# Performance work log

Hardware: AMD Instinct MI355X
Metric: run time of the kernel (lower is better)

Reference implementation:

```python
import jax, jax.numpy as jnp
import numpy as np

D = 300
L = 5
NUM_ATOMS = 87  # MASK_ATOM_ID + 1
BN_EPS = 1e-5


def setup_inputs() -> dict:
    key = jax.random.key(0)
    ks = jax.random.split(key, 24)
    N, E, G = 100000, 250000, 4096
    s = 0.05
    inp = {
        'z': jax.random.randint(ks[0], (N,), 0, 86),
        'chirality': jax.random.uniform(ks[1], (N,), jnp.float32),
        'formal_charge': jax.random.normal(ks[2], (N,), jnp.float32),
        'edge_index': jax.random.randint(ks[3], (2, E), 0, N),
        'edge_attr': jax.random.normal(ks[4], (E, 3), jnp.float32),
        'batch': jnp.sort(jax.random.randint(ks[5], (N,), 0, G)),
        'num_graphs': G,
        # parameters
        'atom_emb': jax.random.normal(ks[6], (NUM_ATOMS, D), jnp.float32) * s,
        'nW1': jax.random.normal(ks[7], (2, D), jnp.float32) * s,
        'nb1': jnp.zeros((D,), jnp.float32),
        'nW2': jax.random.normal(ks[8], (D, D), jnp.float32) * s,
        'nb2': jnp.zeros((D,), jnp.float32),
        'eW1': jax.random.normal(ks[9], (3, D), jnp.float32) * s,
        'eb1': jnp.zeros((D,), jnp.float32),
        'eW2': jax.random.normal(ks[10], (D, D), jnp.float32) * s,
        'eb2': jnp.zeros((D,), jnp.float32),
        'mW1': jax.random.normal(ks[11], (L, D, D), jnp.float32) * s,
        'mb1': jnp.zeros((L, D), jnp.float32),
        'mW2': jax.random.normal(ks[12], (L, D, D), jnp.float32) * s,
        'mb2': jnp.zeros((L, D), jnp.float32),
        'gamma': jnp.ones((L, D), jnp.float32),
        'beta': jnp.zeros((L, D), jnp.float32),
        'pW': jax.random.normal(ks[13], (D, D), jnp.float32) * s,
        'pb': jnp.zeros((D,), jnp.float32),
    }
    return inp


def _mlp2(x, W1, b1, W2, b2):
    return jax.nn.relu(x @ W1 + b1) @ W2 + b2


def reference(z, chirality, formal_charge, edge_index, edge_attr, batch, num_graphs,
              atom_emb, nW1, nb1, nW2, nb2, eW1, eb1, eW2, eb2,
              mW1, mb1, mW2, mb2, gamma, beta, pW, pb):
    N = z.shape[0]
    # node features: atom embedding + projected (chirality, formal_charge)
    node_attr = jnp.stack([chirality, formal_charge], axis=-1)  # [N,2]
    x = atom_emb[z] + _mlp2(node_attr, nW1, nb1, nW2, nb2)      # [N,D]
    # edge features: encode 3-d bond attrs to D (edge_proj is Identity since dims match)
    e = _mlp2(edge_attr, eW1, eb1, eW2, eb2)                    # [E,D]
    src, dst = edge_index[0], edge_index[1]
    h = x
    for l in range(L):
        # GINEConv: mlp((1+eps)*x_i + sum_j relu(x_j + e_ij)), eps=0
        msg = jax.nn.relu(h[src] + e)                           # [E,D] gather
        agg = jax.ops.segment_sum(msg, dst, num_segments=N)     # [N,D] scatter-add
        h2 = _mlp2(h + agg, mW1[l], mb1[l], mW2[l], mb2[l])
        # BatchNorm1d (training stats over nodes, biased var)
        mu = jnp.mean(h2, axis=0)
        var = jnp.var(h2, axis=0)
        h2 = (h2 - mu) * jax.lax.rsqrt(var + BN_EPS) * gamma[l] + beta[l]
        h = jax.nn.relu(h2)
    # per-graph mean pooling
    sums = jax.ops.segment_sum(h, batch, num_segments=num_graphs)      # [G,D]
    counts = jax.ops.segment_sum(jnp.ones((N,), h.dtype), batch, num_segments=num_graphs)
    pooled = sums / jnp.maximum(counts, 1.0)[:, None]
    return pooled @ pW + pb
```

## Files before the change

### kernel.cpp

```cpp
#include <hip/hip_runtime.h>

#define DD 300
#define KP 320
#define WTR 384

typedef __attribute__((ext_vector_type(8))) short short8v;
typedef __attribute__((ext_vector_type(4))) float f32x4;

__device__ __forceinline__ float4 ld4(const float* p) { return *(const float4*)p; }

__device__ __forceinline__ unsigned short f2bf(float f) {
    unsigned int u = __float_as_uint(f);
    unsigned int r = (u + 0x7fffu + ((u >> 16) & 1u)) >> 16;
    return (unsigned short)r;
}
__device__ __forceinline__ float bf2f(unsigned short b) {
    return __uint_as_float(((unsigned int)b) << 16);
}

__device__ __forceinline__ void gload16(const void* g, void* l) {
    __builtin_amdgcn_global_load_lds(
        (const __attribute__((address_space(1))) unsigned int*)g,
        (__attribute__((address_space(3))) unsigned int*)l, 16, 0, 0);
}

__device__ __forceinline__ unsigned char f2e4(float f) {
    unsigned int u = __float_as_uint(f);
    unsigned int s = (u >> 24) & 0x80u;
    float a = __uint_as_float(u & 0x7fffffffu);
    if (a >= 448.f) return (unsigned char)(s | 0x7Eu);
    if (a < 0x1p-10f) return (unsigned char)s;
    int e = (int)((__float_as_uint(a) >> 23) & 0xFF) - 127;
    int q = (e >= -6) ? (e - 3) : -9;
    float scale = __uint_as_float((unsigned int)(127 - q) << 23);
    int m = __float2int_rn(a * scale);
    if (e >= -6) {
        if (m == 16) { m = 8; e += 1; }
        return (unsigned char)(s | ((unsigned int)(e + 7) << 3) | (unsigned int)(m - 8));
    } else {
        if (m == 8) return (unsigned char)(s | (1u << 3));
        return (unsigned char)(s | (unsigned int)m);
    }
}
__device__ __forceinline__ float e42f(unsigned char b) {
    unsigned int s = ((unsigned int)(b & 0x80u)) << 24;
    unsigned int ef = (b >> 3) & 0xFu, mf = b & 7u;
    float mag = (ef == 0) ? ((float)mf) * 0x1p-9f
                          : __uint_as_float(((ef + 120u) << 23) | (mf << 20));
    return __uint_as_float(__float_as_uint(mag) | s);
}

__global__ void prep_all(const float* __restrict__ nW2, const float* __restrict__ eW2,
                         const float* __restrict__ mW1, const float* __restrict__ mW2,
                         unsigned short* __restrict__ wt,
                         double* __restrict__ bnsum, double* __restrict__ bnsq)
{
    const int per = WTR * KP;
    int id = blockIdx.x * 256 + threadIdx.x;
    if (id < 12 * per) {
        int m = id / per, r = id - m * per;
        int col = r / KP, k = r - col * KP;
        const float* W = (m == 0) ? nW2 : (m == 1) ? eW2
                       : (m < 7) ? (mW1 + (size_t)(m - 2) * DD * DD)
                                 : (mW2 + (size_t)(m - 7) * DD * DD);
        float v = (col < DD && k < DD) ? W[(size_t)k * DD + col] : 0.f;
        unsigned short h = f2bf(v);
        wt[(size_t)m * 2 * per + (size_t)col * KP + k] = h;
        wt[(size_t)m * 2 * per + per + (size_t)col * KP + k] = f2bf(v - bf2f(h));
    } else if (id < 12 * per + DD) {
        int c = id - 12 * per;
        bnsum[c] = 0.0; bnsq[c] = 0.0;
    }
}

enum { MA_DMA2 = 0, MA_BF16 = 1, MA_NODE = 2, MA_EDGE = 3 };
enum { ME_RELU = 0, ME_BN = 1, ME_EMB = 2, ME_FP8 = 3 };

constexpr int TM = 256;
constexpr int TN = 128;
constexpr int TK = 32;
constexpr int KSTEPS = 10;

template<int AM, int EM>
__launch_bounds__(512)
__global__ void mgemm(const unsigned short* __restrict__ Aa,
                      const unsigned short* __restrict__ Ab,
                      const unsigned short* __restrict__ Bth,
                      const unsigned short* __restrict__ Btl,
                      const float* __restrict__ bias,
                      const float* __restrict__ W1,
                      const float* __restrict__ b1,
                      const int* __restrict__ zidx,
                      const float* __restrict__ emb,
                      const int* __restrict__ permpos,
                      void* __restrict__ Cv,
                      double* __restrict__ bnsum, double* __restrict__ bnsq,
                      int M)
{
    constexpr bool VSTAGE = (AM == MA_NODE || AM == MA_EDGE);
    constexpr bool ALO    = (AM == MA_NODE);
    constexpr int  AP     = VSTAGE ? 40 : 32;
    __shared__ unsigned short sAh[TM * AP];
    __shared__ unsigned short sBh[TN * 32];
    __shared__ unsigned short sBl[TN * 32];
    __shared__ unsigned short sA2[(AM == MA_DMA2) ? TM * 32 : 64];
    __shared__ unsigned short sAl[ALO ? TM * 40 : 64];

    const int t    = threadIdx.x;
    const int col0 = blockIdx.x * TN;
    const int row0 = blockIdx.y * TM;
    const int lane = t & 63;
    const int wid  = t >> 6;
    const int wr   = wid >> 1;
    const int wc   = wid & 1;
    const int lr   = lane & 15;
    const int lk   = lane >> 4;

    const int arow = t >> 1;
    const int akq  = (t & 1) * 16;
    const int dmarow = lane >> 2;
    const int dmakq  = (lane & 3) * 8;
    const int wbA  = wid * 32;
    const int wbB  = wid * 16;

    const int ga = row0 + arow;
    float f0 = 0.f, f1 = 0.f, f2 = 0.f;
    if (AM == MA_NODE && ga < M) {
        f0 = ((const float*)Aa)[ga]; f1 = ((const float*)Ab)[ga];
    }
    if (AM == MA_EDGE && ga < M) {
        const float* Af = (const float*)Aa;
        f0 = Af[(size_t)ga * 3 + 0];
        f1 = Af[(size_t)ga * 3 + 1];
        f2 = Af[(size_t)ga * 3 + 2];
    }

    f32x4 acc[4][4];
#pragma unroll
    for (int i = 0; i < 4; ++i)
#pragma unroll
        for (int j = 0; j < 4; ++j) acc[i][j] = (f32x4){0.f, 0.f, 0.f, 0.f};

    for (int ks = 0; ks < KSTEPS; ++ks) {
        const int k0 = ks * TK;
        __syncthreads();

        gload16(Bth + (size_t)(col0 + wbB + dmarow) * KP + k0 + dmakq, &sBh[wbB * 32]);
        gload16(Btl + (size_t)(col0 + wbB + dmarow) * KP + k0 + dmakq, &sBl[wbB * 32]);

        if (AM == MA_DMA2) {
#pragma unroll
            for (int i = 0; i < 2; ++i) {
                const int rb = wbA + i * 16;
                gload16(Aa + (size_t)(row0 + rb + dmarow) * DD + k0 + dmakq, &sAh[rb * 32]);
                gload16(Ab + (size_t)(row0 + rb + dmarow) * DD + k0 + dmakq, &sA2[rb * 32]);
            }
        } else if (AM == MA_BF16) {
#pragma unroll
            for (int i = 0; i < 2; ++i) {
                const int rb = wbA + i * 16;
                gload16(Aa + (size_t)(row0 + rb + dmarow) * DD + k0 + dmakq, &sAh[rb * 32]);
            }
        } else {
            float v[16];
#pragma unroll
            for (int q = 0; q < 4; ++q) {
                const int k = k0 + akq + q * 4;
                if (ga < M && k < DD) {
                    float4 w0 = ld4(W1 + k);
                    float4 w1 = ld4(W1 + DD + k);
                    float4 bb = ld4(b1 + k);
                    if (AM == MA_NODE) {
                        v[q*4+0] = fmaxf(fmaf(f0, w0.x, fmaf(f1, w1.x, bb.x)), 0.f);
                        v[q*4+1] = fmaxf(fmaf(f0, w0.y, fmaf(f1, w1.y, bb.y)), 0.f);
                        v[q*4+2] = fmaxf(fmaf(f0, w0.z, fmaf(f1, w1.z, bb.z)), 0.f);
                        v[q*4+3] = fmaxf(fmaf(f0, w0.w, fmaf(f1, w1.w, bb.w)), 0.f);
                    } else {
                        float4 w2 = ld4(W1 + 2 * DD + k);
                        v[q*4+0] = fmaxf(f0*w0.x + f1*w1.x + f2*w2.x + bb.x, 0.f);
                        v[q*4+1] = fmaxf(f0*w0.y + f1*w1.y + f2*w2.y + bb.y, 0.f);
                        v[q*4+2] = fmaxf(f0*w0.z + f1*w1.z + f2*w2.z + bb.z, 0.f);
                        v[q*4+3] = fmaxf(f0*w0.w + f1*w1.w + f2*w2.w + bb.w, 0.f);
                    }
                } else {
                    v[q*4+0] = v[q*4+1] = v[q*4+2] = v[q*4+3] = 0.f;
                }
            }
#pragma unroll
            for (int q = 0; q < 4; ++q) {
                ushort4 hi;
                hi.x = f2bf(v[q*4+0]);
                hi.y = f2bf(v[q*4+1]);
                hi.z = f2bf(v[q*4+2]);
                hi.w = f2bf(v[q*4+3]);
                *(ushort4*)&sAh[arow * AP + akq + q * 4] = hi;
                if constexpr (ALO) {
                    ushort4 lo;
                    lo.x = f2bf(v[q*4+0] - bf2f(hi.x));
                    lo.y = f2bf(v[q*4+1] - bf2f(hi.y));
                    lo.z = f2bf(v[q*4+2] - bf2f(hi.z));
                    lo.w = f2bf(v[q*4+3] - bf2f(hi.w));
                    *(ushort4*)&sAl[arow * 40 + akq + q * 4] = lo;
                }
            }
        }
        __syncthreads();

        short8v aH[4], aX[4], bH[4], bL[4];
#pragma unroll
        for (int f = 0; f < 4; ++f) {
            aH[f] = *(const short8v*)&sAh[(wr * 64 + f * 16 + lr) * AP + lk * 8];
            bH[f] = *(const short8v*)&sBh[(wc * 64 + f * 16 + lr) * 32 + lk * 8];
            bL[f] = *(const short8v*)&sBl[(wc * 64 + f * 16 + lr) * 32 + lk * 8];
            if constexpr (AM == MA_DMA2)
                aX[f] = *(const short8v*)&sA2[(wr * 64 + f * 16 + lr) * 32 + lk * 8];
            if constexpr (ALO)
                aX[f] = *(const short8v*)&sAl[(wr * 64 + f * 16 + lr) * 40 + lk * 8];
        }
#pragma unroll
        for (int fi = 0; fi < 4; ++fi)
#pragma unroll
            for (int fj = 0; fj < 4; ++fj) {
                acc[fi][fj] = __builtin_amdgcn_mfma_f32_16x16x32_bf16(aH[fi], bH[fj], acc[fi][fj], 0, 0, 0);
                acc[fi][fj] = __builtin_amdgcn_mfma_f32_16x16x32_bf16(aH[fi], bL[fj], acc[fi][fj], 0, 0, 0);
                if constexpr (AM == MA_DMA2) {
                    acc[fi][fj] = __builtin_amdgcn_mfma_f32_16x16x32_bf16(aX[fi], bH[fj], acc[fi][fj], 0, 0, 0);
                    acc[fi][fj] = __builtin_amdgcn_mfma_f32_16x16x32_bf16(aX[fi], bL[fj], acc[fi][fj], 0, 0, 0);
                }
                if constexpr (ALO)
                    acc[fi][fj] = __builtin_amdgcn_mfma_f32_16x16x32_bf16(aX[fi], bH[fj], acc[fi][fj], 0, 0, 0);
            }
    }

    float csum[4], csq[4];
#pragma unroll
    for (int j = 0; j < 4; ++j) { csum[j] = 0.f; csq[j] = 0.f; }

#pragma unroll
    for (int fi = 0; fi < 4; ++fi) {
#pragma unroll
        for (int i = 0; i < 4; ++i) {
            const int r = row0 + wr * 64 + fi * 16 + lk * 4 + i;
            if (r < M) {
                int zr = 0, pr = 0;
                if (EM == ME_EMB) zr = zidx[r];
                if (EM == ME_FP8) pr = permpos[r];
#pragma unroll
                for (int fj = 0; fj < 4; ++fj) {
                    const int c = col0 + wc * 64 + fj * 16 + lr;
                    if (c < DD) {
                        float v = acc[fi][fj][i] + bias[c];
                        if (EM == ME_RELU) v = fmaxf(v, 0.f);
                        if (EM == ME_EMB)  v += emb[(size_t)zr * DD + c];
                        if (EM == ME_FP8)
                            ((unsigned char*)Cv)[(size_t)pr * DD + c] = f2e4(v);
                        else
                            ((unsigned short*)Cv)[(size_t)r * DD + c] = f2bf(v);
                        if (EM == ME_BN) { csum[fj] += v; csq[fj] += v * v; }
                    }
                }
            }
        }
    }

    if (EM == ME_BN) {
#pragma unroll
        for (int fj = 0; fj < 4; ++fj) {
            csum[fj] += __shfl_xor(csum[fj], 16);
            csum[fj] += __shfl_xor(csum[fj], 32);
            csq[fj]  += __shfl_xor(csq[fj], 16);
            csq[fj]  += __shfl_xor(csq[fj], 32);
        }
        float* sRed = (float*)sAh;
        __syncthreads();
        if (lk == 0) {
#pragma unroll
            for (int fj = 0; fj < 4; ++fj)
                sRed[wr * TN + wc * 64 + fj * 16 + lr] = csum[fj];
        }
        __syncthreads();
        if (t < TN) {
            float s = sRed[t] + sRed[TN + t] + sRed[2 * TN + t] + sRed[3 * TN + t];
            const int c = col0 + t;
            if (c < DD) unsafeAtomicAdd(&bnsum[c], (double)s);
        }
        __syncthreads();
        if (lk == 0) {
#pragma unroll
            for (int fj = 0; fj < 4; ++fj)
                sRed[wr * TN + wc * 64 + fj * 16 + lr] = csq[fj];
        }
        __syncthreads();
        if (t < TN) {
            float s = sRed[t] + sRed[TN + t] + sRed[2 * TN + t] + sRed[3 * TN + t];
            const int c = col0 + t;
            if (c < DD) unsafeAtomicAdd(&bnsq[c], (double)s);
        }
    }
}

constexpr int GBM = 128;
constexpr int GBN = 128;
constexpr int GBK = 8;
constexpr int KPAD = 304;

__launch_bounds__(256)
__global__ void gemm_final(const float* __restrict__ Aa, const float* __restrict__ Bw,
                           const float* __restrict__ bias, float* __restrict__ C, int M)
{
    __shared__ float smem[2 * GBK * GBM];
    float* As = smem;
    float* Bs = smem + GBK * GBM;

    const int t    = threadIdx.x;
    const int tx   = t & 15;
    const int ty   = t >> 4;
    const int col0 = blockIdx.x * GBN;
    const int row0 = blockIdx.y * GBM;
    const int arow = t >> 1;
    const int akq  = (t & 1) << 2;
    const int brow = t >> 5;
    const int bnq  = (t & 31) << 2;
    const int ga   = row0 + arow;
    const int gb   = col0 + bnq;

    float acc[8][8];
#pragma unroll
    for (int i = 0; i < 8; ++i)
#pragma unroll
        for (int j = 0; j < 8; ++j) acc[i][j] = 0.f;

    for (int k0 = 0; k0 < KPAD; k0 += GBK) {
        float4 av = make_float4(0.f, 0.f, 0.f, 0.f);
        const int ka = k0 + akq;
        if (ga < M && ka < DD) av = ld4(Aa + (size_t)ga * DD + ka);
        As[(akq + 0) * GBM + arow] = av.x;
        As[(akq + 1) * GBM + arow] = av.y;
        As[(akq + 2) * GBM + arow] = av.z;
        As[(akq + 3) * GBM + arow] = av.w;

        float4 bv = make_float4(0.f, 0.f, 0.f, 0.f);
        const int kb = k0 + brow;
        if (kb < DD && gb < DD) bv = ld4(Bw + (size_t)kb * DD + gb);
        *(float4*)(Bs + brow * GBN + bnq) = bv;

        __syncthreads();
#pragma unroll
        for (int kk = 0; kk < GBK; ++kk) {
            float a[8], b[8];
            *(float4*)&a[0] = *(const float4*)(As + kk * GBM + 8 * ty);
            *(float4*)&a[4] = *(const float4*)(As + kk * GBM + 8 * ty + 4);
            *(float4*)&b[0] = *(const float4*)(Bs + kk * GBN + 8 * tx);
            *(float4*)&b[4] = *(const float4*)(Bs + kk * GBN + 8 * tx + 4);
#pragma unroll
            for (int i = 0; i < 8; ++i)
#pragma unroll
                for (int j = 0; j < 8; ++j)
                    acc[i][j] = fmaf(a[i], b[j], acc[i][j]);
        }
        __syncthreads();
    }

#pragma unroll
    for (int i = 0; i < 8; ++i) {
        const int r = row0 + 8 * ty + i;
        if (r < M) {
#pragma unroll
            for (int jq = 0; jq < 2; ++jq) {
                const int c = col0 + 8 * tx + 4 * jq;
                if (c < DD) {
                    float4 bb = ld4(bias + c);
                    *(float4*)(C + (size_t)r * DD + c) = make_float4(
                        acc[i][4*jq+0] + bb.x, acc[i][4*jq+1] + bb.y,
                        acc[i][4*jq+2] + bb.z, acc[i][4*jq+3] + bb.w);
                }
            }
        }
    }
}

__global__ void deg_kernel(const int* __restrict__ dst, int* __restrict__ deg, int E)
{
    int e = blockIdx.x * 256 + threadIdx.x;
    if (e < E) atomicAdd(&deg[dst[e]], 1);
}

__global__ void scan1(const int* __restrict__ deg, int* __restrict__ out,
                      int* __restrict__ bsum, int n)
{
    __shared__ int sh[256];
    const int t = threadIdx.x;
    const int base = blockIdx.x * 1024 + t * 4;
    int v0 = (base + 0 < n) ? deg[base + 0] : 0;
    int v1 = (base + 1 < n) ? deg[base + 1] : 0;
    int v2 = (base + 2 < n) ? deg[base + 2] : 0;
    int v3 = (base + 3 < n) ? deg[base + 3] : 0;
    const int s = v0 + v1 + v2 + v3;
    sh[t] = s;
    __syncthreads();
    for (int off = 1; off < 256; off <<= 1) {
        int x = (t >= off) ? sh[t - off] : 0;
        __syncthreads();
        sh[t] += x;
        __syncthreads();
    }
    int ex = sh[t] - s;
    if (base + 0 < n) out[base + 0] = ex; ex += v0;
    if (base + 1 < n) out[base + 1] = ex; ex += v1;
    if (base + 2 < n) out[base + 2] = ex; ex += v2;
    if (base + 3 < n) out[base + 3] = ex;
    if (t == 255) bsum[blockIdx.x] = sh[255];
}

__global__ void scan2(int* __restrict__ bsum, int nb, int* __restrict__ offs, int n, int E)
{
    __shared__ int sh[256];
    const int t = threadIdx.x;
    const int v = (t < nb) ? bsum[t] : 0;
    sh[t] = v;
    __syncthreads();
    for (int off = 1; off < 256; off <<= 1) {
        int x = (t >= off) ? sh[t - off] : 0;
        __syncthreads();
        sh[t] += x;
        __syncthreads();
    }
    if (t < nb) bsum[t] = sh[t] - v;
    if (t == 0) offs[n] = E;
}

__global__ void scan3(int* __restrict__ offs, const int* __restrict__ bsum,
                      int* __restrict__ cursor, int n)
{
    int i = blockIdx.x * 256 + threadIdx.x;
    if (i < n) {
        int v = offs[i] + bsum[i >> 10];
        offs[i] = v;
        cursor[i] = v;
    }
}

__global__ void fill_kernel(const int* __restrict__ src, const int* __restrict__ dst,
                            int* __restrict__ cursor, int* __restrict__ esrc,
                            int* __restrict__ permpos, int E)
{
    int e = blockIdx.x * 256 + threadIdx.x;
    if (e < E) {
        int d = dst[e];
        int pos = atomicAdd(&cursor[d], 1);
        esrc[pos] = src[e];
        permpos[e] = pos;
    }
}

__global__ void agg_kernel(const unsigned short* __restrict__ h,
                           const unsigned char* __restrict__ e,
                           const int* __restrict__ esrc, const int* __restrict__ offs,
                           unsigned short* __restrict__ agg, int N)
{
    const int node = blockIdx.x * 4 + (threadIdx.x >> 6);
    if (node >= N) return;
    const int lane = threadIdx.x & 63;
    const int beg = offs[node], end = offs[node + 1];
    for (int q = lane; q < 75; q += 64) {
        float4 s = make_float4(0.f, 0.f, 0.f, 0.f);
        for (int p = beg; p < end; ++p) {
            const int src = esrc[p];
            ushort4 hu = *(const ushort4*)(h + (size_t)src * DD + 4 * q);
            unsigned int eu = *(const unsigned int*)(e + (size_t)p * DD + 4 * q);
            s.x += fmaxf(bf2f(hu.x) + e42f((unsigned char)(eu & 0xFF)), 0.f);
            s.y += fmaxf(bf2f(hu.y) + e42f((unsigned char)((eu >> 8) & 0xFF)), 0.f);
            s.z += fmaxf(bf2f(hu.z) + e42f((unsigned char)((eu >> 16) & 0xFF)), 0.f);
            s.w += fmaxf(bf2f(hu.w) + e42f((unsigned char)(eu >> 24)), 0.f);
        }
        *(ushort4*)(agg + (size_t)node * DD + 4 * q) =
            make_ushort4(f2bf(s.x), f2bf(s.y), f2bf(s.z), f2bf(s.w));
    }
}

__global__ void bn_fin(double* __restrict__ bnsum, double* __restrict__ bnsq,
                       const float* __restrict__ gamma, const float* __restrict__ beta,
                       float* __restrict__ scale, float* __restrict__ shift, double invN)
{
    const int c = threadIdx.x;
    if (c < DD) {
        double mu = bnsum[c] * invN;
        double var = bnsq[c] * invN - mu * mu;
        double inv = 1.0 / sqrt(var + 1e-5);
        double g = (double)gamma[c];
        scale[c] = (float)(g * inv);
        shift[c] = (float)((double)beta[c] - mu * inv * g);
        bnsum[c] = 0.0;
        bnsq[c]  = 0.0;
    }
}

__global__ void bn_apply(const unsigned short* __restrict__ h2,
                         const float* __restrict__ scale, const float* __restrict__ shift,
                         unsigned short* __restrict__ h, int total4)
{
    int idx = blockIdx.x * 256 + threadIdx.x;
    if (idx >= total4) return;
    int q = idx % 75;
    ushort4 v4 = ((const ushort4*)h2)[idx];
    float4 sc = ld4(scale + 4 * q);
    float4 sh = ld4(shift + 4 * q);
    float r0 = fmaxf(fmaf(bf2f(v4.x), sc.x, sh.x), 0.f);
    float r1 = fmaxf(fmaf(bf2f(v4.y), sc.y, sh.y), 0.f);
    float r2 = fmaxf(fmaf(bf2f(v4.z), sc.z, sh.z), 0.f);
    float r3 = fmaxf(fmaf(bf2f(v4.w), sc.w, sh.w), 0.f);
    ((ushort4*)h)[idx] = make_ushort4(f2bf(r0), f2bf(r1), f2bf(r2), f2bf(r3));
}

__global__ void pool_kernel(const unsigned short* __restrict__ h, const int* __restrict__ batch,
                            float* __restrict__ pooled, int N)
{
    const int g = blockIdx.x;
    __shared__ int sb[2];
    if (threadIdx.x == 0) {
        int lo = 0, hi = N;
        while (lo < hi) { int m = (lo + hi) >> 1; if (batch[m] < g) lo = m + 1; else hi = m; }
        sb[0] = lo;
        lo = 0; hi = N;
        while (lo < hi) { int m = (lo + hi) >> 1; if (batch[m] < g + 1) lo = m + 1; else hi = m; }
        sb[1] = lo;
    }
    __syncthreads();
    const int beg = sb[0], end = sb[1];
    const float cnt = (float)(end - beg);
    for (int d = threadIdx.x; d < DD; d += 256) {
        float s = 0.f;
        for (int i = beg; i < end; ++i) s += bf2f(h[(size_t)i * DD + d]);
        pooled[(size_t)g * DD + d] = (end > beg) ? (s / cnt) : 0.f;
    }
}

__global__ void diag_fill(float* __restrict__ out, int n, float v)
{
    int i = blockIdx.x * 256 + threadIdx.x;
    if (i < n) out[i] = v;
}

extern "C" void kernel_launch(void* const* d_in, const int* in_sizes, int n_in,
                              void* d_out, int out_size, void* d_ws, size_t ws_size,
                              hipStream_t stream)
{
    const int N = in_sizes[0];
    const int E = in_sizes[3] / 2;
    const int G = out_size / DD;
    const int NPAD = (N + 255) & ~255;

    const int*   z     = (const int*)d_in[0];
    const float* chir  = (const float*)d_in[1];
    const float* fc    = (const float*)d_in[2];
    const int*   eidx  = (const int*)d_in[3];
    const float* eattr = (const float*)d_in[4];
    const int*   batch = (const int*)d_in[5];
    const float* aemb  = (const float*)d_in[7];
    const float* nW1   = (const float*)d_in[8];
    const float* nb1   = (const float*)d_in[9];
    const float* nW2   = (const float*)d_in[10];
    const float* nb2   = (const float*)d_in[11];
    const float* eW1   = (const float*)d_in[12];
    const float* eb1   = (const float*)d_in[13];
    const float* eW2   = (const float*)d_in[14];
    const float* eb2   = (const float*)d_in[15];
    const float* mW1   = (const float*)d_in[16];
    const float* mb1   = (const float*)d_in[17];
    const float* mW2   = (const float*)d_in[18];
    const float* mb2   = (const float*)d_in[19];
    const float* gamma = (const float*)d_in[20];
    const float* beta  = (const float*)d_in[21];
    const float* pW    = (const float*)d_in[22];
    const float* pb    = (const float*)d_in[23];
    float* out = (float*)d_out;

    size_t base = 0;
    auto A = [&](size_t b) -> size_t {
        size_t r = base; base += (b + 255) & ~(size_t)255; return r;
    };
    const size_t o_h    = A((size_t)NPAD * DD * 2 + 128);
    const size_t o_t    = A((size_t)NPAD * DD * 2 + 128);
    const size_t o_g    = A((size_t)NPAD * DD * 2 + 128);
    const size_t o_bns  = A(DD * 8);
    const size_t o_bnq  = A(DD * 8);
    const size_t o_scl  = A(DD * 4);
    const size_t o_shf  = A(DD * 4);
    const size_t o_offs = A((size_t)(N + 1) * 4);
    const size_t o_cur  = A((size_t)N * 4);
    const size_t o_bsum = A(1024 * 4);
    const size_t o_src  = A((size_t)E * 4);
    const size_t o_perm = A((size_t)E * 4);
    const size_t o_wt   = A((size_t)12 * 2 * WTR * KP * 2);
    const size_t o_e    = A((size_t)E * DD * 1);
    const size_t need = base;

    if (ws_size < need) {
        diag_fill<<<(out_size + 255) / 256, 256, 0, stream>>>(
            out, out_size, 10000.f + (float)(ws_size >> 20));
        return;
    }

    char* w = (char*)d_ws;
    unsigned short* h      = (unsigned short*)(w + o_h);
    unsigned short* tbuf   = (unsigned short*)(w + o_t);
    unsigned short* aggh2  = (unsigned short*)(w + o_g);
    double*         bnsum  = (double*)(w + o_bns);
    double*         bnsq   = (double*)(w + o_bnq);
    float*          scl    = (float*)(w + o_scl);
    float*          shf    = (float*)(w + o_shf);
    int*            offs   = (int*)(w + o_offs);
    int*            cursor = (int*)(w + o_cur);
    int*            bsum   = (int*)(w + o_bsum);
    int*            esrc   = (int*)(w + o_src);
    int*            permpos= (int*)(w + o_perm);
    unsigned short* wt     = (unsigned short*)(w + o_wt);
    unsigned char*  ebuf   = (unsigned char*)(w + o_e);
    float*          pooled = (float*)tbuf;

    const size_t per = (size_t)WTR * KP;
    auto wHI = [&](int m) { return wt + (size_t)m * 2 * per; };
    auto wLO = [&](int m) { return wt + (size_t)m * 2 * per + per; };

    const int* srcI = eidx;
    const int* dstI = eidx + E;

    const int ptot = 12 * WTR * KP + DD;
    prep_all<<<(ptot + 255) / 256, 256, 0, stream>>>(nW2, eW2, mW1, mW2, wt, bnsum, bnsq);

    hipMemsetAsync(cursor, 0, (size_t)N * 4, stream);
    deg_kernel<<<(E + 255) / 256, 256, 0, stream>>>(dstI, cursor, E);
    const int nb = (N + 1023) / 1024;
    scan1<<<nb, 256, 0, stream>>>(cursor, offs, bsum, N);
    scan2<<<1, 256, 0, stream>>>(bsum, nb, offs, N, E);
    scan3<<<(N + 255) / 256, 256, 0, stream>>>(offs, bsum, cursor, N);
    fill_kernel<<<(E + 255) / 256, 256, 0, stream>>>(srcI, dstI, cursor, esrc, permpos, E);

    const dim3 gN(3, (N + TM - 1) / TM);
    const dim3 gE(3, (E + TM - 1) / TM);
    const dim3 gG(3, (G + GBM - 1) / GBM);

    mgemm<MA_NODE, ME_EMB><<<gN, 512, 0, stream>>>(
        (const unsigned short*)chir, (const unsigned short*)fc, wHI(0), wLO(0), nb2,
        nW1, nb1, z, aemb, nullptr, h, nullptr, nullptr, N);
    mgemm<MA_EDGE, ME_FP8><<<gE, 512, 0, stream>>>(
        (const unsigned short*)eattr, nullptr, wHI(1), wLO(1), eb2,
        eW1, eb1, nullptr, nullptr, permpos, ebuf, nullptr, nullptr, E);

    for (int l = 0; l < 5; ++l) {
        agg_kernel<<<(N + 3) / 4, 256, 0, stream>>>(h, ebuf, esrc, offs, aggh2, N);
        mgemm<MA_DMA2, ME_RELU><<<gN, 512, 0, stream>>>(
            h, aggh2, wHI(2 + l), wLO(2 + l), mb1 + l * DD,
            nullptr, nullptr, nullptr, nullptr, nullptr, tbuf, nullptr, nullptr, N);
        mgemm<MA_BF16, ME_BN><<<gN, 512, 0, stream>>>(
            tbuf, nullptr, wHI(7 + l), wLO(7 + l), mb2 + l * DD,
            nullptr, nullptr, nullptr, nullptr, nullptr, aggh2, bnsum, bnsq, N);
        bn_fin<<<1, 320, 0, stream>>>(bnsum, bnsq, gamma + l * DD, beta + l * DD,
                                      scl, shf, 1.0 / (double)N);
        const int tot4 = N * 75;
        bn_apply<<<(tot4 + 255) / 256, 256, 0, stream>>>(aggh2, scl, shf, h, tot4);
    }

    pool_kernel<<<G, 256, 0, stream>>>(h, batch, pooled, N);
    gemm_final<<<gG, 256, 0, stream>>>(pooled, pW, pb, out, G);
}
```

Before: 2.625 ms.

## Double-buffer LDS tiles in mgemm to overlap next-K loads with MFMA

Doubles the shared-memory A and B tile buffers and moves tile staging into a lambda. The tile for step k+1 is issued into the alternate buffer right after the barrier, then the MFMAs for step k run. This removes one barrier per K step and lets the global-to-LDS DMA overlap with compute. The cost is twice the LDS per block, which may lower occupancy.

```diff
diff --git a/kernel.cpp b/kernel.cpp
--- a/kernel.cpp
+++ b/kernel.cpp
@@ -100,11 +100,13 @@
     constexpr bool VSTAGE = (AM == MA_NODE || AM == MA_EDGE);
     constexpr bool ALO    = (AM == MA_NODE);
     constexpr int  AP     = VSTAGE ? 40 : 32;
-    __shared__ unsigned short sAh[TM * AP];
-    __shared__ unsigned short sBh[TN * 32];
-    __shared__ unsigned short sBl[TN * 32];
-    __shared__ unsigned short sA2[(AM == MA_DMA2) ? TM * 32 : 64];
-    __shared__ unsigned short sAl[ALO ? TM * 40 : 64];
+    constexpr int  ABUF   = TM * AP;
+    constexpr int  BBUF   = TN * 32;
+    __shared__ unsigned short sAh[2 * ABUF];
+    __shared__ unsigned short sBh[2 * BBUF];
+    __shared__ unsigned short sBl[2 * BBUF];
+    __shared__ unsigned short sA2[(AM == MA_DMA2) ? 2 * ABUF : 64];
+    __shared__ unsigned short sAl[ALO ? 2 * ABUF : 64];
 
     const int t    = threadIdx.x;
     const int col0 = blockIdx.x * TN;
@@ -135,31 +137,26 @@
         f2 = Af[(size_t)ga * 3 + 2];
     }
 
-    f32x4 acc[4][4];
-#pragma unroll
-    for (int i = 0; i < 4; ++i)
-#pragma unroll
-        for (int j = 0; j < 4; ++j) acc[i][j] = (f32x4){0.f, 0.f, 0.f, 0.f};
-
-    for (int ks = 0; ks < KSTEPS; ++ks) {
+    auto STAGE = [&](int ks, int bi) {
         const int k0 = ks * TK;
-        __syncthreads();
-
-        gload16(Bth + (size_t)(col0 + wbB + dmarow) * KP + k0 + dmakq, &sBh[wbB * 32]);
-        gload16(Btl + (size_t)(col0 + wbB + dmarow) * KP + k0 + dmakq, &sBl[wbB * 32]);
-
-        if (AM == MA_DMA2) {
+        unsigned short* dBh = sBh + bi * BBUF;
+        unsigned short* dBl = sBl + bi * BBUF;
+        unsigned short* dAh = sAh + bi * ABUF;
+        gload16(Bth + (size_t)(col0 + wbB + dmarow) * KP + k0 + dmakq, dBh + wbB * 32);
+        gload16(Btl + (size_t)(col0 + wbB + dmarow) * KP + k0 + dmakq, dBl + wbB * 32);
+        if constexpr (AM == MA_DMA2) {
+            unsigned short* dA2 = sA2 + bi * ABUF;
 #pragma unroll
             for (int i = 0; i < 2; ++i) {
                 const int rb = wbA + i * 16;
-                gload16(Aa + (size_t)(row0 + rb + dmarow) * DD + k0 + dmakq, &sAh[rb * 32]);
-                gload16(Ab + (size_t)(row0 + rb + dmarow) * DD + k0 + dmakq, &sA2[rb * 32]);
-            }
-        } else if (AM == MA_BF16) {
+                gload16(Aa + (size_t)(row0 + rb + dmarow) * DD + k0 + dmakq, dAh + rb * 32);
+                gload16(Ab + (size_t)(row0 + rb + dmarow) * DD + k0 + dmakq, dA2 + rb * 32);
+            }
+        } else if constexpr (AM == MA_BF16) {
 #pragma unroll
             for (int i = 0; i < 2; ++i) {
                 const int rb = wbA + i * 16;
-                gload16(Aa + (size_t)(row0 + rb + dmarow) * DD + k0 + dmakq, &sAh[rb * 32]);
+                gload16(Aa + (size_t)(row0 + rb + dmarow) * DD + k0 + dmakq, dAh + rb * 32);
             }
         } else {
             float v[16];
@@ -193,29 +190,49 @@
                 hi.y = f2bf(v[q*4+1]);
                 hi.z = f2bf(v[q*4+2]);
                 hi.w = f2bf(v[q*4+3]);
-                *(ushort4*)&sAh[arow * AP + akq + q * 4] = hi;
+                *(ushort4*)&dAh[arow * AP + akq + q * 4] = hi;
                 if constexpr (ALO) {
+                    unsigned short* dAl = sAl + bi * ABUF;
                     ushort4 lo;
                     lo.x = f2bf(v[q*4+0] - bf2f(hi.x));
                     lo.y = f2bf(v[q*4+1] - bf2f(hi.y));
                     lo.z = f2bf(v[q*4+2] - bf2f(hi.z));
                     lo.w = f2bf(v[q*4+3] - bf2f(hi.w));
-                    *(ushort4*)&sAl[arow * 40 + akq + q * 4] = lo;
+                    *(ushort4*)&dAl[arow * AP + akq + q * 4] = lo;
                 }
             }
         }
-        __syncthreads();
-
+    };
+
+    f32x4 acc[4][4];
+#pragma unroll
+    for (int i = 0; i < 4; ++i)
+#pragma unroll
+        for (int j = 0; j < 4; ++j) acc[i][j] = (f32x4){0.f, 0.f, 0.f, 0.f};
+
+    STAGE(0, 0);
+    for (int ks = 0; ks < KSTEPS; ++ks) {
+        const int bi = ks & 1;
+        __syncthreads();
+        if (ks + 1 < KSTEPS) STAGE(ks + 1, bi ^ 1);
+
+        const unsigned short* rAh = sAh + bi * ABUF;
+        const unsigned short* rBh = sBh + bi * BBUF;
+        const unsigned short* rBl = sBl + bi * BBUF;
         short8v aH[4], aX[4], bH[4], bL[4];
 #pragma unroll
         for (int f = 0; f < 4; ++f) {
-            aH[f] = *(const short8v*)&sAh[(wr * 64 + f * 16 + lr) * AP + lk * 8];
-            bH[f] = *(const short8v*)&sBh[(wc * 64 + f * 16 + lr) * 32 + lk * 8];
-            bL[f] = *(const short8v*)&sBl[(wc * 64 + f * 16 + lr) * 32 + lk * 8];
-            if constexpr (AM == MA_DMA2)
-                aX[f] = *(const short8v*)&sA2[(wr * 64 + f * 16 + lr) * 32 + lk * 8];
-            if constexpr (ALO)
-                aX[f] = *(const short8v*)&sAl[(wr * 64 + f * 16 + lr) * 40 + lk * 8];
+            aH[f] = *(const short8v*)&rAh[(wr * 64 + f * 16 + lr) * AP + lk * 8];
+            bH[f] = *(const short8v*)&rBh[(wc * 64 + f * 16 + lr) * 32 + lk * 8];
+            bL[f] = *(const short8v*)&rBl[(wc * 64 + f * 16 + lr) * 32 + lk * 8];
+            if constexpr (AM == MA_DMA2) {
+                const unsigned short* rA2 = sA2 + bi * ABUF;
+                aX[f] = *(const short8v*)&rA2[(wr * 64 + f * 16 + lr) * 32 + lk * 8];
+            }
+            if constexpr (ALO) {
+                const unsigned short* rAl = sAl + bi * ABUF;
+                aX[f] = *(const short8v*)&rAl[(wr * 64 + f * 16 + lr) * AP + lk * 8];
+            }
         }
 #pragma unroll
         for (int fi = 0; fi < 4; ++fi)
```

Measured after the change: 2.648 ms. Within noise of the previous version (+0.9%).
